# Optimization experiments

Measured on AMD Instinct MI355X. Metric: run time of the kernel, lower is better.

Reference implementation:

```python
import jax, jax.numpy as jnp
import numpy as np

NUM_HEADS = 16
D_IN = 1024
D_OUT = 64  # = D_IN // NUM_HEADS
N = 2048


def setup_inputs() -> dict:
    key = jax.random.key(0)
    kx, kq, kk, kv, ko = jax.random.split(key, 5)
    x = jax.random.normal(kx, (N, D_IN), dtype=jnp.float32)
    # per-head projection weights, stacked over heads (torch code keeps a
    # Python list of SelfAttention modules; stacking is the vectorized form)
    q_proj = jax.random.normal(kq, (NUM_HEADS, D_IN, D_OUT), dtype=jnp.float32)
    k_proj = jax.random.normal(kk, (NUM_HEADS, D_IN, D_OUT), dtype=jnp.float32)
    v_proj = jax.random.normal(kv, (NUM_HEADS, D_IN, D_OUT), dtype=jnp.float32)
    o_proj = jax.random.normal(ko, (D_IN, D_IN), dtype=jnp.float32)
    return {"x": x, "q_proj": q_proj, "k_proj": k_proj, "v_proj": v_proj, "o_proj": o_proj}


def reference(x, q_proj, k_proj, v_proj, o_proj):
    d_out = q_proj.shape[-1]
    # per-head projections: [H, N, E]
    q = jnp.einsum('nd,hde->hne', x, q_proj)
    k = jnp.einsum('nd,hde->hne', x, k_proj)
    v = jnp.einsum('nd,hde->hne', x, v_proj)
    # full NxN scores per head (matches the naive torch implementation's math)
    scores = jnp.einsum('hne,hme->hnm', q, k) / jnp.sqrt(jnp.float32(d_out))
    attn = jax.nn.softmax(scores, axis=-1)
    ctx = jnp.einsum('hnm,hme->hne', attn, v)
    # concat heads along the feature dim (head 0 first, as in torch.cat)
    h, n, e = ctx.shape
    out = jnp.transpose(ctx, (1, 0, 2)).reshape(n, h * e)
    return out @ o_proj
```

## Files before the change

kernel.cpp:

```cpp
#include <hip/hip_runtime.h>

#define H 16
#define N 2048
#define E 64
#define D 1024

typedef __attribute__((ext_vector_type(8))) short bf16x8;
typedef __attribute__((ext_vector_type(4))) float f32x4;

__device__ __forceinline__ float bf2f(unsigned short u) {
    union { unsigned int i; float f; } v;
    v.i = ((unsigned int)u) << 16;
    return v.f;
}
__device__ __forceinline__ unsigned short f2bf(float f) {
    unsigned int u = __float_as_uint(f);
    return (unsigned short)((u + 0x7fffu + ((u >> 16) & 1u)) >> 16);
}
#define MFMA(a, b, c) __builtin_amdgcn_mfma_f32_16x16x32_bf16(a, b, c, 0, 0, 0)

typedef __attribute__((address_space(3))) unsigned int lds_u32;
typedef const __attribute__((address_space(1))) unsigned int glb_u32;
__device__ __forceinline__ void dma16(const unsigned short* g, unsigned short* l) {
    __builtin_amdgcn_global_load_lds((glb_u32*)g, (lds_u32*)l, 16, 0, 0);
}

__device__ __forceinline__ int sw8(int row, int c)  { return row * 64  + ((c ^ (row & 7)) << 3); }
__device__ __forceinline__ int sw16(int row, int c) { return row * 128 + ((c ^ (row & 7)) << 3); }

__global__ __launch_bounds__(256) void convert_x_kernel(
    const float* __restrict__ x, unsigned short* __restrict__ xh,
    unsigned short* __restrict__ xl)
{
    const int i = (blockIdx.x * 256 + threadIdx.x) * 4;
    const float4 v = *(const float4*)&x[i];
    ushort4 hh, ll;
    hh.x = f2bf(v.x); ll.x = f2bf(v.x - bf2f(hh.x));
    hh.y = f2bf(v.y); ll.y = f2bf(v.y - bf2f(hh.y));
    hh.z = f2bf(v.z); ll.z = f2bf(v.z - bf2f(hh.z));
    hh.w = f2bf(v.w); ll.w = f2bf(v.w - bf2f(hh.w));
    *(ushort4*)&xh[i] = hh;
    *(ushort4*)&xl[i] = ll;
}

__global__ __launch_bounds__(256) void convert_w_kernel(
    const float* __restrict__ qw, const float* __restrict__ kw,
    const float* __restrict__ vw, const float* __restrict__ ow,
    unsigned short* __restrict__ wBh, unsigned short* __restrict__ wBl,
    unsigned short* __restrict__ wvt,
    unsigned short* __restrict__ woh, unsigned short* __restrict__ wol)
{
    __shared__ float ts[64][65];
    const int b = blockIdx.x;
    const int t = threadIdx.x;
    const float* src;
    int rs, dt, orow0;
    bool has_lo;
    unsigned short *dh, *dl;
    if (b < 768) {
        const int which = b >> 8, r = b & 255, h = r >> 4;
        dt = r & 15;
        src = (which == 0 ? qw : which == 1 ? kw : vw) + ((size_t)h * D + dt * 64) * E;
        rs = E;
        if (which == 0)      { dh = wBh; dl = wBl; orow0 = h * 64;        has_lo = true; }
        else if (which == 1) { dh = wBh; dl = wBl; orow0 = 1024 + h * 64; has_lo = true; }
        else                 { dh = wvt; dl = wBl; orow0 = h * 64;        has_lo = false; }
    } else {
        const int r = b - 768, ct = r >> 4;
        dt = r & 15;
        src = ow + (size_t)(dt * 64) * D + ct * 64;
        rs = D;
        orow0 = ct * 64;
        dh = woh; dl = wol; has_lo = true;
    }
    {
        const int row = t >> 2, cb = (t & 3) * 16;
        #pragma unroll
        for (int j = 0; j < 16; j += 4) {
            const float4 v = *(const float4*)&src[row * rs + cb + j];
            ts[row][cb + j + 0] = v.x;
            ts[row][cb + j + 1] = v.y;
            ts[row][cb + j + 2] = v.z;
            ts[row][cb + j + 3] = v.w;
        }
    }
    __syncthreads();
    {
        const int cl = t >> 2, dp = (t & 3) * 16;
        bf16x8 hv0, hv1, lv0, lv1;
        #pragma unroll
        for (int i = 0; i < 16; ++i) {
            const float f = ts[dp + i][cl];
            const unsigned short hh = f2bf(f);
            const unsigned short lo = f2bf(f - bf2f(hh));
            if (i < 8) { hv0[i] = (short)hh; lv0[i] = (short)lo; }
            else       { hv1[i - 8] = (short)hh; lv1[i - 8] = (short)lo; }
        }
        const size_t o = (size_t)(orow0 + cl) * D + dt * 64 + dp;
        *(bf16x8*)&dh[o] = hv0;
        *(bf16x8*)&dh[o + 8] = hv1;
        if (has_lo) {
            *(bf16x8*)&dl[o] = lv0;
            *(bf16x8*)&dl[o + 8] = lv1;
        }
    }
}

__global__ __launch_bounds__(256, 3) void qkv_kernel(
    const unsigned short* __restrict__ xh, const unsigned short* __restrict__ xl,
    const unsigned short* __restrict__ wBh, const unsigned short* __restrict__ wBl,
    const unsigned short* __restrict__ wvt,
    unsigned short* __restrict__ Qh, unsigned short* __restrict__ Ql,
    unsigned short* __restrict__ Kh, unsigned short* __restrict__ Kl,
    unsigned short* __restrict__ Vt)
{
    __shared__ unsigned short ash[128 * 64], asl[128 * 64];
    __shared__ unsigned short bsh[64 * 64], bsl[64 * 64];
    const int n0 = blockIdx.x * 128;
    const int ct0 = blockIdx.y;
    const int sec = ct0 >> 4;
    const int hh = ct0 & 15;
    const bool isv = (sec == 2);
    const unsigned short* Bh = isv ? wvt : wBh;
    const size_t brow0 = (sec == 1 ? 1024 : 0) + hh * 64;

    const int t = threadIdx.x;
    const int lane = t & 63, wvi = t >> 6, quad = lane >> 4, l15 = lane & 15;

    f32x4 acc[2][4];
    #pragma unroll
    for (int i = 0; i < 2; ++i)
        #pragma unroll
        for (int j = 0; j < 4; ++j) acc[i][j] = (f32x4){0.f, 0.f, 0.f, 0.f};

    for (int k0 = 0; k0 < D; k0 += 64) {
        __syncthreads();
        #pragma unroll
        for (int p = 0; p < 4; ++p) {
            const int row = p * 32 + wvi * 8 + (lane >> 3);
            const int lc = (lane & 7) ^ (row & 7);
            const int lo = p * 2048 + wvi * 512 + lane * 8;
            const size_t ga = (size_t)(n0 + row) * D + k0 + lc * 8;
            dma16(&xh[ga], &ash[lo]);
            if (!isv) dma16(&xl[ga], &asl[lo]);
        }
        #pragma unroll
        for (int p = 0; p < 2; ++p) {
            const int row = p * 32 + wvi * 8 + (lane >> 3);
            const int lc = (lane & 7) ^ (row & 7);
            const int lo = p * 2048 + wvi * 512 + lane * 8;
            const size_t gb = (brow0 + row) * D + k0 + lc * 8;
            dma16(&Bh[gb], &bsh[lo]);
            if (!isv) dma16(&wBl[gb], &bsl[lo]);
        }
        __syncthreads();

        #pragma unroll
        for (int kwi = 0; kwi < 2; ++kwi) {
            const int c = kwi * 4 + quad;
            bf16x8 ah[2], al[2], bh[4], bl[4];
            #pragma unroll
            for (int i = 0; i < 2; ++i) {
                ah[i] = *(const bf16x8*)&ash[sw8(wvi * 32 + i * 16 + l15, c)];
                if (!isv) al[i] = *(const bf16x8*)&asl[sw8(wvi * 32 + i * 16 + l15, c)];
            }
            #pragma unroll
            for (int j = 0; j < 4; ++j) {
                bh[j] = *(const bf16x8*)&bsh[sw8(j * 16 + l15, c)];
                if (!isv) bl[j] = *(const bf16x8*)&bsl[sw8(j * 16 + l15, c)];
            }
            #pragma unroll
            for (int i = 0; i < 2; ++i)
                #pragma unroll
                for (int j = 0; j < 4; ++j) {
                    acc[i][j] = MFMA(ah[i], bh[j], acc[i][j]);
                    if (!isv) {
                        acc[i][j] = MFMA(ah[i], bl[j], acc[i][j]);
                        acc[i][j] = MFMA(al[i], bh[j], acc[i][j]);
                    }
                }
        }
    }

    if (isv) {
        #pragma unroll
        for (int j = 0; j < 4; ++j) {
            const int e = j * 16 + l15;
            #pragma unroll
            for (int i = 0; i < 2; ++i) {
                const int nb = n0 + wvi * 32 + i * 16 + quad * 4;
                ushort4 pk;
                pk.x = f2bf(acc[i][j][0]);
                pk.y = f2bf(acc[i][j][1]);
                pk.z = f2bf(acc[i][j][2]);
                pk.w = f2bf(acc[i][j][3]);
                *(ushort4*)&Vt[((size_t)hh * 64 + e) * N + nb] = pk;
            }
        }
    } else {
        const float scale = (sec == 0) ? 0.125f : 1.0f;
        unsigned short* Oh = (sec == 0) ? Qh : Kh;
        unsigned short* Ol = (sec == 0) ? Ql : Kl;
        #pragma unroll
        for (int j = 0; j < 4; ++j) {
            const int e = j * 16 + l15;
            #pragma unroll
            for (int i = 0; i < 2; ++i)
                #pragma unroll
                for (int r = 0; r < 4; ++r) {
                    const int n = n0 + wvi * 32 + i * 16 + quad * 4 + r;
                    const float val = acc[i][j][r] * scale;
                    const unsigned short hv = f2bf(val);
                    Oh[((size_t)hh * N + n) * E + e] = hv;
                    Ol[((size_t)hh * N + n) * E + e] = f2bf(val - bf2f(hv));
                }
        }
    }
}

__global__ __launch_bounds__(256, 2) void attn_kernel(
    const unsigned short* __restrict__ Qh, const unsigned short* __restrict__ Ql,
    const unsigned short* __restrict__ Kh, const unsigned short* __restrict__ Kl,
    const unsigned short* __restrict__ Vt,
    unsigned short* __restrict__ Ch, unsigned short* __restrict__ Cl)
{
    __shared__ unsigned short ksh[128 * 64], ksl[128 * 64];
    __shared__ unsigned short vts[64 * 128];
    __shared__ unsigned short ps[4 * 16 * 136];
    const int r0 = blockIdx.x * 64, h = blockIdx.y;
    const int t = threadIdx.x, lane = t & 63, wvi = t >> 6, quad = lane >> 4, l15 = lane & 15;

    bf16x8 qfh[2], qfl[2];
    {
        const size_t base = ((size_t)h * N + r0 + wvi * 16 + l15) * E;
        #pragma unroll
        for (int kwi = 0; kwi < 2; ++kwi) {
            qfh[kwi] = *(const bf16x8*)&Qh[base + kwi * 32 + quad * 8];
            qfl[kwi] = *(const bf16x8*)&Ql[base + kwi * 32 + quad * 8];
        }
    }

    f32x4 oacc[4];
    #pragma unroll
    for (int ct = 0; ct < 4; ++ct) oacc[ct] = (f32x4){0.f, 0.f, 0.f, 0.f};
    float mrow[4] = {-1e30f, -1e30f, -1e30f, -1e30f};
    float lrow[4] = {0.f, 0.f, 0.f, 0.f};

    for (int m0 = 0; m0 < N; m0 += 128) {
        __syncthreads();
        #pragma unroll
        for (int p = 0; p < 4; ++p) {
            const int row = p * 32 + wvi * 8 + (lane >> 3);
            const int lc = (lane & 7) ^ (row & 7);
            const int lo = p * 2048 + wvi * 512 + lane * 8;
            const size_t gk = ((size_t)h * N + m0 + row) * E + lc * 8;
            dma16(&Kh[gk], &ksh[lo]);
            dma16(&Kl[gk], &ksl[lo]);
        }
        #pragma unroll
        for (int p = 0; p < 4; ++p) {
            const int row = p * 16 + wvi * 4 + (lane >> 4);
            const int lc = (lane & 15) ^ (row & 7);
            const int lo = p * 2048 + wvi * 512 + lane * 8;
            dma16(&Vt[((size_t)h * 64 + row) * N + m0 + lc * 8], &vts[lo]);
        }
        __syncthreads();

        f32x4 s[8];
        #pragma unroll
        for (int ct = 0; ct < 8; ++ct) s[ct] = (f32x4){0.f, 0.f, 0.f, 0.f};
        #pragma unroll
        for (int kwi = 0; kwi < 2; ++kwi) {
            const int c = kwi * 4 + quad;
            #pragma unroll
            for (int ct = 0; ct < 8; ++ct) {
                const bf16x8 bh = *(const bf16x8*)&ksh[sw8(ct * 16 + l15, c)];
                const bf16x8 bl = *(const bf16x8*)&ksl[sw8(ct * 16 + l15, c)];
                s[ct] = MFMA(qfh[kwi], bh, s[ct]);
                s[ct] = MFMA(qfh[kwi], bl, s[ct]);
                s[ct] = MFMA(qfl[kwi], bh, s[ct]);
            }
        }

        #pragma unroll
        for (int r = 0; r < 4; ++r) {
            float mx = s[0][r];
            #pragma unroll
            for (int ct = 1; ct < 8; ++ct) mx = fmaxf(mx, s[ct][r]);
            mx = fmaxf(mx, __shfl_xor(mx, 1));
            mx = fmaxf(mx, __shfl_xor(mx, 2));
            mx = fmaxf(mx, __shfl_xor(mx, 4));
            mx = fmaxf(mx, __shfl_xor(mx, 8));
            const float mn = fmaxf(mrow[r], mx);
            const float alpha = __expf(mrow[r] - mn);
            mrow[r] = mn;
            float sum = 0.f;
            #pragma unroll
            for (int ct = 0; ct < 8; ++ct) {
                const float p = __expf(s[ct][r] - mn);
                s[ct][r] = p;
                sum += p;
            }
            sum += __shfl_xor(sum, 1);
            sum += __shfl_xor(sum, 2);
            sum += __shfl_xor(sum, 4);
            sum += __shfl_xor(sum, 8);
            lrow[r] = lrow[r] * alpha + sum;
            #pragma unroll
            for (int ct = 0; ct < 4; ++ct) oacc[ct][r] *= alpha;
        }

        #pragma unroll
        for (int ct = 0; ct < 8; ++ct)
            #pragma unroll
            for (int r = 0; r < 4; ++r)
                ps[(wvi * 16 + quad * 4 + r) * 136 + ct * 16 + l15] = f2bf(s[ct][r]);

        #pragma unroll
        for (int kwi = 0; kwi < 4; ++kwi) {
            const bf16x8 pa = *(const bf16x8*)&ps[(wvi * 16 + l15) * 136 + kwi * 32 + quad * 8];
            #pragma unroll
            for (int ct = 0; ct < 4; ++ct) {
                const bf16x8 vb = *(const bf16x8*)&vts[sw16(ct * 16 + l15, kwi * 4 + quad)];
                oacc[ct] = MFMA(pa, vb, oacc[ct]);
            }
        }
    }

    #pragma unroll
    for (int r = 0; r < 4; ++r) {
        const float inv = 1.f / lrow[r];
        const int n = r0 + wvi * 16 + quad * 4 + r;
        #pragma unroll
        for (int ct = 0; ct < 4; ++ct) {
            const int c = h * 64 + ct * 16 + l15;
            const float val = oacc[ct][r] * inv;
            const unsigned short hv = f2bf(val);
            Ch[(size_t)n * D + c] = hv;
            Cl[(size_t)n * D + c] = f2bf(val - bf2f(hv));
        }
    }
}

__global__ __launch_bounds__(256, 2) void out_proj_kernel(
    const unsigned short* __restrict__ Chh, const unsigned short* __restrict__ Cll,
    const unsigned short* __restrict__ Wh, const unsigned short* __restrict__ Wl,
    float* __restrict__ out)
{
    __shared__ unsigned short ash[64 * 64], asl[64 * 64];
    __shared__ unsigned short bsh[64 * 64], bsl[64 * 64];
    const int n0 = blockIdx.x * 64, c0 = blockIdx.y * 64;
    const int t = threadIdx.x, lane = t & 63, wvi = t >> 6, quad = lane >> 4, l15 = lane & 15;

    f32x4 acc[4];
    #pragma unroll
    for (int j = 0; j < 4; ++j) acc[j] = (f32x4){0.f, 0.f, 0.f, 0.f};

    for (int k0 = 0; k0 < D; k0 += 64) {
        __syncthreads();
        #pragma unroll
        for (int p = 0; p < 2; ++p) {
            const int row = p * 32 + wvi * 8 + (lane >> 3);
            const int lc = (lane & 7) ^ (row & 7);
            const int lo = p * 2048 + wvi * 512 + lane * 8;
            const size_t ga = (size_t)(n0 + row) * D + k0 + lc * 8;
            const size_t gb = (size_t)(c0 + row) * D + k0 + lc * 8;
            dma16(&Chh[ga], &ash[lo]);
            dma16(&Cll[ga], &asl[lo]);
            dma16(&Wh[gb], &bsh[lo]);
            dma16(&Wl[gb], &bsl[lo]);
        }
        __syncthreads();

        #pragma unroll
        for (int kwi = 0; kwi < 2; ++kwi) {
            const int c = kwi * 4 + quad;
            const bf16x8 ah = *(const bf16x8*)&ash[sw8(wvi * 16 + l15, c)];
            const bf16x8 al = *(const bf16x8*)&asl[sw8(wvi * 16 + l15, c)];
            #pragma unroll
            for (int j = 0; j < 4; ++j) {
                const bf16x8 bh = *(const bf16x8*)&bsh[sw8(j * 16 + l15, c)];
                const bf16x8 bl = *(const bf16x8*)&bsl[sw8(j * 16 + l15, c)];
                acc[j] = MFMA(ah, bh, acc[j]);
                acc[j] = MFMA(ah, bl, acc[j]);
                acc[j] = MFMA(al, bh, acc[j]);
            }
        }
    }

    #pragma unroll
    for (int r = 0; r < 4; ++r) {
        const int n = n0 + wvi * 16 + quad * 4 + r;
        #pragma unroll
        for (int j = 0; j < 4; ++j)
            out[(size_t)n * D + c0 + j * 16 + l15] = acc[j][r];
    }
}

extern "C" void kernel_launch(void* const* d_in, const int* in_sizes, int n_in,
                              void* d_out, int out_size, void* d_ws, size_t ws_size,
                              hipStream_t stream) {
    const float* x  = (const float*)d_in[0];
    const float* qw = (const float*)d_in[1];
    const float* kw = (const float*)d_in[2];
    const float* vw = (const float*)d_in[3];
    const float* ow = (const float*)d_in[4];
    float* out = (float*)d_out;

    unsigned short* ws = (unsigned short*)d_ws;
    const size_t M1 = 1024 * 1024;
    unsigned short* wBh = ws;
    unsigned short* wBl = ws + 2 * M1;
    unsigned short* wvt = ws + 4 * M1;
    unsigned short* woh = ws + 5 * M1;
    unsigned short* wol = ws + 6 * M1;
    unsigned short* xh  = ws + 7 * M1;
    unsigned short* xl  = ws + 9 * M1;
    unsigned short* Qh  = ws + 11 * M1;
    unsigned short* Ql  = ws + 13 * M1;
    unsigned short* Kh  = ws + 15 * M1;
    unsigned short* Kl  = ws + 17 * M1;
    unsigned short* Vt  = ws + 19 * M1;
    unsigned short* Ch  = xh;
    unsigned short* Cl  = xl;

    convert_x_kernel<<<(N * D / 4) / 256, 256, 0, stream>>>(x, xh, xl);
    convert_w_kernel<<<1024, 256, 0, stream>>>(qw, kw, vw, ow, wBh, wBl, wvt, woh, wol);
    qkv_kernel<<<dim3(16, 48), 256, 0, stream>>>(xh, xl, wBh, wBl, wvt, Qh, Ql, Kh, Kl, Vt);
    attn_kernel<<<dim3(32, 16), 256, 0, stream>>>(Qh, Ql, Kh, Kl, Vt, Ch, Cl);
    out_proj_kernel<<<dim3(32, 16), 256, 0, stream>>>(Ch, Cl, woh, wol, out);
}
```

Baseline: 191.0 us.

## Enlarge QKV and out-proj GEMM tiles to 128x128, split-K out-proj with atomics

The QKV projection now uses 128x128 output tiles, where it used 128x64 tiles, so the grid drops from 48 to 24 column blocks and each wave computes a 64x64 quadrant with more operand reuse. The output projection moves from 64x64 tiles to 128x128 tiles with a 2-way split over K, and the partial sums are accumulated into a zero-initialised output with float atomicAdd. Larger tiles cut global and LDS traffic per MFMA but raise register and LDS use, and launch bounds drop to 2 blocks per SM. The atomics and the extra memset add write traffic and make the summation order non-deterministic.

Result: slower. 210.8 us (+10.3%).

```diff
diff --git a/kernel.cpp b/kernel.cpp
--- a/kernel.cpp
+++ b/kernel.cpp
@@ -106,7 +106,7 @@
     }
 }
 
-__global__ __launch_bounds__(256, 3) void qkv_kernel(
+__global__ __launch_bounds__(256, 2) void qkv_kernel(
     const unsigned short* __restrict__ xh, const unsigned short* __restrict__ xl,
     const unsigned short* __restrict__ wBh, const unsigned short* __restrict__ wBl,
     const unsigned short* __restrict__ wvt,
@@ -115,21 +115,20 @@
     unsigned short* __restrict__ Vt)
 {
     __shared__ unsigned short ash[128 * 64], asl[128 * 64];
-    __shared__ unsigned short bsh[64 * 64], bsl[64 * 64];
+    __shared__ unsigned short bsh[128 * 64], bsl[128 * 64];
     const int n0 = blockIdx.x * 128;
-    const int ct0 = blockIdx.y;
-    const int sec = ct0 >> 4;
-    const int hh = ct0 & 15;
-    const bool isv = (sec == 2);
+    const int by = blockIdx.y;
+    const bool isv = (by >= 16);
     const unsigned short* Bh = isv ? wvt : wBh;
-    const size_t brow0 = (sec == 1 ? 1024 : 0) + hh * 64;
+    const size_t brow0 = isv ? (size_t)(by - 16) * 128 : (size_t)by * 128;
 
     const int t = threadIdx.x;
     const int lane = t & 63, wvi = t >> 6, quad = lane >> 4, l15 = lane & 15;
-
-    f32x4 acc[2][4];
+    const int qr = (wvi >> 1) * 64, qc = (wvi & 1) * 64;
+
+    f32x4 acc[4][4];
     #pragma unroll
-    for (int i = 0; i < 2; ++i)
+    for (int i = 0; i < 4; ++i)
         #pragma unroll
         for (int j = 0; j < 4; ++j) acc[i][j] = (f32x4){0.f, 0.f, 0.f, 0.f};
 
@@ -141,36 +140,31 @@
             const int lc = (lane & 7) ^ (row & 7);
             const int lo = p * 2048 + wvi * 512 + lane * 8;
             const size_t ga = (size_t)(n0 + row) * D + k0 + lc * 8;
+            const size_t gb = (brow0 + row) * D + k0 + lc * 8;
             dma16(&xh[ga], &ash[lo]);
-            if (!isv) dma16(&xl[ga], &asl[lo]);
-        }
-        #pragma unroll
-        for (int p = 0; p < 2; ++p) {
-            const int row = p * 32 + wvi * 8 + (lane >> 3);
-            const int lc = (lane & 7) ^ (row & 7);
-            const int lo = p * 2048 + wvi * 512 + lane * 8;
-            const size_t gb = (brow0 + row) * D + k0 + lc * 8;
             dma16(&Bh[gb], &bsh[lo]);
-            if (!isv) dma16(&wBl[gb], &bsl[lo]);
+            if (!isv) {
+                dma16(&xl[ga], &asl[lo]);
+                dma16(&wBl[gb], &bsl[lo]);
+            }
         }
         __syncthreads();
 
         #pragma unroll
         for (int kwi = 0; kwi < 2; ++kwi) {
             const int c = kwi * 4 + quad;
-            bf16x8 ah[2], al[2], bh[4], bl[4];
-            #pragma unroll
-            for (int i = 0; i < 2; ++i) {
-                ah[i] = *(const bf16x8*)&ash[sw8(wvi * 32 + i * 16 + l15, c)];
-                if (!isv) al[i] = *(const bf16x8*)&asl[sw8(wvi * 32 + i * 16 + l15, c)];
-            }
-            #pragma unroll
-            for (int j = 0; j < 4; ++j) {
-                bh[j] = *(const bf16x8*)&bsh[sw8(j * 16 + l15, c)];
-                if (!isv) bl[j] = *(const bf16x8*)&bsl[sw8(j * 16 + l15, c)];
-            }
-            #pragma unroll
-            for (int i = 0; i < 2; ++i)
+            bf16x8 ah[4], al[4], bh[4], bl[4];
+            #pragma unroll
+            for (int i = 0; i < 4; ++i) {
+                ah[i] = *(const bf16x8*)&ash[sw8(qr + i * 16 + l15, c)];
+                bh[i] = *(const bf16x8*)&bsh[sw8(qc + i * 16 + l15, c)];
+                if (!isv) {
+                    al[i] = *(const bf16x8*)&asl[sw8(qr + i * 16 + l15, c)];
+                    bl[i] = *(const bf16x8*)&bsl[sw8(qc + i * 16 + l15, c)];
+                }
+            }
+            #pragma unroll
+            for (int i = 0; i < 4; ++i)
                 #pragma unroll
                 for (int j = 0; j < 4; ++j) {
                     acc[i][j] = MFMA(ah[i], bh[j], acc[i][j]);
@@ -185,30 +179,32 @@
     if (isv) {
         #pragma unroll
         for (int j = 0; j < 4; ++j) {
-            const int e = j * 16 + l15;
-            #pragma unroll
-            for (int i = 0; i < 2; ++i) {
-                const int nb = n0 + wvi * 32 + i * 16 + quad * 4;
+            const int vcol = (by - 16) * 128 + qc + j * 16 + l15;
+            #pragma unroll
+            for (int i = 0; i < 4; ++i) {
+                const int nb = n0 + qr + i * 16 + quad * 4;
                 ushort4 pk;
                 pk.x = f2bf(acc[i][j][0]);
                 pk.y = f2bf(acc[i][j][1]);
                 pk.z = f2bf(acc[i][j][2]);
                 pk.w = f2bf(acc[i][j][3]);
-                *(ushort4*)&Vt[((size_t)hh * 64 + e) * N + nb] = pk;
+                *(ushort4*)&Vt[(size_t)vcol * N + nb] = pk;
             }
         }
     } else {
-        const float scale = (sec == 0) ? 0.125f : 1.0f;
-        unsigned short* Oh = (sec == 0) ? Qh : Kh;
-        unsigned short* Ol = (sec == 0) ? Ql : Kl;
+        const bool isq = (by < 8);
+        const float scale = isq ? 0.125f : 1.0f;
+        unsigned short* Oh = isq ? Qh : Kh;
+        unsigned short* Ol = isq ? Ql : Kl;
         #pragma unroll
         for (int j = 0; j < 4; ++j) {
-            const int e = j * 16 + l15;
-            #pragma unroll
-            for (int i = 0; i < 2; ++i)
+            const int fcol = (by & 7) * 128 + qc + j * 16 + l15;
+            const int hh = fcol >> 6, e = fcol & 63;
+            #pragma unroll
+            for (int i = 0; i < 4; ++i)
                 #pragma unroll
                 for (int r = 0; r < 4; ++r) {
-                    const int n = n0 + wvi * 32 + i * 16 + quad * 4 + r;
+                    const int n = n0 + qr + i * 16 + quad * 4 + r;
                     const float val = acc[i][j][r] * scale;
                     const unsigned short hv = f2bf(val);
                     Oh[((size_t)hh * N + n) * E + e] = hv;
@@ -347,19 +343,23 @@
     const unsigned short* __restrict__ Wh, const unsigned short* __restrict__ Wl,
     float* __restrict__ out)
 {
-    __shared__ unsigned short ash[64 * 64], asl[64 * 64];
-    __shared__ unsigned short bsh[64 * 64], bsl[64 * 64];
-    const int n0 = blockIdx.x * 64, c0 = blockIdx.y * 64;
+    __shared__ unsigned short ash[128 * 64], asl[128 * 64];
+    __shared__ unsigned short bsh[128 * 64], bsl[128 * 64];
+    const int n0 = blockIdx.x * 128, c0 = blockIdx.y * 128;
+    const int kbase = blockIdx.z * 512;
     const int t = threadIdx.x, lane = t & 63, wvi = t >> 6, quad = lane >> 4, l15 = lane & 15;
-
-    f32x4 acc[4];
+    const int qr = (wvi >> 1) * 64, qc = (wvi & 1) * 64;
+
+    f32x4 acc[4][4];
     #pragma unroll
-    for (int j = 0; j < 4; ++j) acc[j] = (f32x4){0.f, 0.f, 0.f, 0.f};
-
-    for (int k0 = 0; k0 < D; k0 += 64) {
-        __syncthreads();
-        #pragma unroll
-        for (int p = 0; p < 2; ++p) {
+    for (int i = 0; i < 4; ++i)
+        #pragma unroll
+        for (int j = 0; j < 4; ++j) acc[i][j] = (f32x4){0.f, 0.f, 0.f, 0.f};
+
+    for (int k0 = kbase; k0 < kbase + 512; k0 += 64) {
+        __syncthreads();
+        #pragma unroll
+        for (int p = 0; p < 4; ++p) {
             const int row = p * 32 + wvi * 8 + (lane >> 3);
             const int lc = (lane & 7) ^ (row & 7);
             const int lo = p * 2048 + wvi * 512 + lane * 8;
@@ -375,26 +375,34 @@
         #pragma unroll
         for (int kwi = 0; kwi < 2; ++kwi) {
             const int c = kwi * 4 + quad;
-            const bf16x8 ah = *(const bf16x8*)&ash[sw8(wvi * 16 + l15, c)];
-            const bf16x8 al = *(const bf16x8*)&asl[sw8(wvi * 16 + l15, c)];
-            #pragma unroll
-            for (int j = 0; j < 4; ++j) {
-                const bf16x8 bh = *(const bf16x8*)&bsh[sw8(j * 16 + l15, c)];
-                const bf16x8 bl = *(const bf16x8*)&bsl[sw8(j * 16 + l15, c)];
-                acc[j] = MFMA(ah, bh, acc[j]);
-                acc[j] = MFMA(ah, bl, acc[j]);
-                acc[j] = MFMA(al, bh, acc[j]);
-            }
+            bf16x8 ah[4], al[4], bh[4], bl[4];
+            #pragma unroll
+            for (int i = 0; i < 4; ++i) {
+                ah[i] = *(const bf16x8*)&ash[sw8(qr + i * 16 + l15, c)];
+                al[i] = *(const bf16x8*)&asl[sw8(qr + i * 16 + l15, c)];
+                bh[i] = *(const bf16x8*)&bsh[sw8(qc + i * 16 + l15, c)];
+                bl[i] = *(const bf16x8*)&bsl[sw8(qc + i * 16 + l15, c)];
+            }
+            #pragma unroll
+            for (int i = 0; i < 4; ++i)
+                #pragma unroll
+                for (int j = 0; j < 4; ++j) {
+                    acc[i][j] = MFMA(ah[i], bh[j], acc[i][j]);
+                    acc[i][j] = MFMA(ah[i], bl[j], acc[i][j]);
+                    acc[i][j] = MFMA(al[i], bh[j], acc[i][j]);
+                }
         }
     }
 
     #pragma unroll
-    for (int r = 0; r < 4; ++r) {
-        const int n = n0 + wvi * 16 + quad * 4 + r;
-        #pragma unroll
-        for (int j = 0; j < 4; ++j)
-            out[(size_t)n * D + c0 + j * 16 + l15] = acc[j][r];
-    }
+    for (int i = 0; i < 4; ++i)
+        #pragma unroll
+        for (int r = 0; r < 4; ++r) {
+            const int n = n0 + qr + i * 16 + quad * 4 + r;
+            #pragma unroll
+            for (int j = 0; j < 4; ++j)
+                atomicAdd(&out[(size_t)n * D + c0 + qc + j * 16 + l15], acc[i][j][r]);
+        }
 }
 
 extern "C" void kernel_launch(void* const* d_in, const int* in_sizes, int n_in,
@@ -424,9 +432,10 @@
     unsigned short* Ch  = xh;
     unsigned short* Cl  = xl;
 
+    hipMemsetAsync(out, 0, (size_t)out_size * sizeof(float), stream);
     convert_x_kernel<<<(N * D / 4) / 256, 256, 0, stream>>>(x, xh, xl);
     convert_w_kernel<<<1024, 256, 0, stream>>>(qw, kw, vw, ow, wBh, wBl, wvt, woh, wol);
-    qkv_kernel<<<dim3(16, 48), 256, 0, stream>>>(xh, xl, wBh, wBl, wvt, Qh, Ql, Kh, Kl, Vt);
+    qkv_kernel<<<dim3(16, 24), 256, 0, stream>>>(xh, xl, wBh, wBl, wvt, Qh, Ql, Kh, Kl, Vt);
     attn_kernel<<<dim3(32, 16), 256, 0, stream>>>(Qh, Ql, Kh, Kl, Vt, Ch, Cl);
-    out_proj_kernel<<<dim3(32, 16), 256, 0, stream>>>(Ch, Cl, woh, wol, out);
-}
+    out_proj_kernel<<<dim3(16, 8, 2), 256, 0, stream>>>(Ch, Cl, woh, wol, out);
+}
```
